# Optimization experiments

Measured on AMD Instinct MI355X. Metric: run time of the kernel, lower is better.

The kernel has to match this reference:

```python
import jax, jax.numpy as jnp
import numpy as np

NUM_HEADS = 16
HEAD_DIM = 64
EMBED_DIM = 1024
NEG_INF = -1e9
LENGTHS = np.array([1024, 512, 768, 896, 1024, 640, 384, 896], dtype=np.int32)


def rotate_half(x):
    d = x.shape[-1] // 2
    return jnp.concatenate([-x[..., d:], x[..., :d]], axis=-1)


def setup_inputs() -> dict:
    key = jax.random.key(0)
    ks = jax.random.split(key, 8)
    E, H, Dh = EMBED_DIM, NUM_HEADS, HEAD_DIM
    T = int(LENGTHS.sum())  # 6144 packed tokens
    hidden_states = jax.random.normal(ks[0], (T, E), jnp.float32)
    # RoPE tables: positions restart at 0 for each packed segment
    pos = np.concatenate([np.arange(l) for l in LENGTHS]).astype(np.float32)
    inv_freq = 1.0 / (10000.0 ** (np.arange(0, Dh, 2, dtype=np.float32) / Dh))
    freqs = pos[:, None] * inv_freq[None, :]           # [T, Dh/2]
    emb = np.concatenate([freqs, freqs], axis=-1)       # [T, Dh]
    cos = jnp.asarray(np.cos(emb), jnp.float32)
    sin = jnp.asarray(np.sin(emb), jnp.float32)
    s = 0.02
    Wq = jax.random.normal(ks[1], (E, E), jnp.float32) * s
    Wk = jax.random.normal(ks[2], (E, E), jnp.float32) * s
    Wv = jax.random.normal(ks[3], (E, E), jnp.float32) * s
    Wo = jax.random.normal(ks[4], (E, E), jnp.float32) * s
    bq = jnp.zeros((E,), jnp.float32)
    bv = jnp.zeros((E,), jnp.float32)
    bo = jnp.zeros((E,), jnp.float32)
    return dict(hidden_states=hidden_states, seq_len=jnp.asarray(LENGTHS),
                cos=cos, sin=sin, Wq=Wq, bq=bq, Wk=Wk, Wv=Wv, bv=bv, Wo=Wo, bo=bo)


def reference(hidden_states, seq_len, cos, sin, Wq, bq, Wk, Wv, bv, Wo, bo):
    T, E = hidden_states.shape
    H, Dh = NUM_HEADS, HEAD_DIM
    # q/k/v projections (k_proj has no bias, matching nn.Linear(bias=False))
    q = (hidden_states @ Wq.T + bq).reshape(T, H, Dh)
    k = (hidden_states @ Wk.T).reshape(T, H, Dh)
    v = (hidden_states @ Wv.T + bv).reshape(T, H, Dh)
    # rotary embedding, cos/sin broadcast over heads
    c = cos[:, None, :]
    s = sin[:, None, :]
    q = q * c + rotate_half(q) * s
    k = k * c + rotate_half(k) * s
    # unpack ragged -> padded [B, Lmax, H, Dh] (indices are static wrt data)
    lens = np.asarray(seq_len)
    B = lens.shape[0]
    Lmax = int(lens.max())
    cu = np.concatenate([[0], np.cumsum(lens)])
    pad_idx = cu[:-1, None] + np.arange(Lmax)[None, :]   # [B, Lmax]
    valid = np.arange(Lmax)[None, :] < lens[:, None]     # [B, Lmax]
    pad_idx = np.where(valid, pad_idx, 0)
    qp = q[pad_idx]  # [B, Lmax, H, Dh]
    kp = k[pad_idx]
    vp = v[pad_idx]
    # attention with causal + key-padding mask (equivalent to per-segment loop)
    scores = jnp.einsum('bqhd,bkhd->bhqk', qp, kp) / np.sqrt(Dh).astype(np.float32)
    causal = np.tril(np.ones((Lmax, Lmax), dtype=bool))
    mask = causal[None, None, :, :] & valid[:, None, None, :]
    scores = jnp.where(mask, scores, NEG_INF)
    probs = jax.nn.softmax(scores, axis=-1)
    out = jnp.einsum('bhqk,bkhd->bqhd', probs, vp).reshape(B, Lmax, E)
    # repack padded -> [T, E]
    b_ids = np.repeat(np.arange(B), lens)
    l_ids = np.concatenate([np.arange(l) for l in lens])
    packed = out[b_ids, l_ids]
    return packed @ Wo.T + bo
```

## Files before the change

### kernel.cpp

```cpp
#include <hip/hip_runtime.h>
#include <stdint.h>

typedef __bf16 bf16;
typedef __bf16 bf16x8 __attribute__((ext_vector_type(8)));
typedef __bf16 bf16x4 __attribute__((ext_vector_type(4)));
typedef float f32x4 __attribute__((ext_vector_type(4)));

#define T_TOT 6144
#define E_DIM 1024
#define NHEAD 16

__device__ __forceinline__ void gload16(const void* g, void* l) {
    __builtin_amdgcn_global_load_lds((const __attribute__((address_space(1))) void*)g,
                                     (__attribute__((address_space(3))) void*)l, 16, 0, 0);
}

__global__ __launch_bounds__(256) void cvt_all_kernel(const float* __restrict__ hs,
        const float* __restrict__ wq, const float* __restrict__ wk,
        const float* __restrict__ wv, const float* __restrict__ wo,
        bf16* __restrict__ hsb, bf16* __restrict__ wqb, bf16* __restrict__ wkb,
        bf16* __restrict__ wvb, bf16* __restrict__ wob) {
    const size_t TE = (size_t)T_TOT * E_DIM;
    const size_t EE = (size_t)E_DIM * E_DIM;
    size_t i = ((size_t)blockIdx.x * 256 + threadIdx.x) * 4;
    const float* src; bf16* dst; size_t off;
    if (i < TE)               { src = hs; dst = hsb; off = i; }
    else if (i < TE + EE)     { src = wq; dst = wqb; off = i - TE; }
    else if (i < TE + 2 * EE) { src = wk; dst = wkb; off = i - TE - EE; }
    else if (i < TE + 3 * EE) { src = wv; dst = wvb; off = i - TE - 2 * EE; }
    else                      { src = wo; dst = wob; off = i - TE - 3 * EE; }
    float4 v = *reinterpret_cast<const float4*>(src + off);
    union { bf16 h[4]; uint2 u; } pk;
    pk.h[0] = (bf16)v.x; pk.h[1] = (bf16)v.y; pk.h[2] = (bf16)v.z; pk.h[3] = (bf16)v.w;
    *reinterpret_cast<uint2*>(dst + off) = pk.u;
}

__global__ __launch_bounds__(256, 2) void qkv_gemm_kernel(
        const bf16* __restrict__ hsb,
        const bf16* __restrict__ wq, const bf16* __restrict__ wk, const bf16* __restrict__ wv,
        const float* __restrict__ bq, const float* __restrict__ bv,
        const float* __restrict__ cosb, const float* __restrict__ sinb,
        bf16* __restrict__ qo, bf16* __restrict__ ko, bf16* __restrict__ vto) {
    __shared__ bf16 As[192 * 64];
    __shared__ bf16 Bs[128 * 64];

    const int b    = blockIdx.x;
    const int swzi = (b & 7) * 96 + (b >> 3);
    const int bn   = swzi & 7;
    const int t1   = swzi >> 3;
    const int bm   = t1 & 31;
    const int z    = t1 >> 5;
    const bf16*  W    = (z == 0) ? wq : (z == 1) ? wk : wv;
    const float* bias = (z == 0) ? bq : (z == 1) ? nullptr : bv;

    const int tid  = threadIdx.x;
    const int lane = tid & 63;
    const int wid  = tid >> 6;
    const int l15  = lane & 15, l4 = lane >> 4;
    const int wr   = wid >> 1, wc = wid & 1;

    f32x4 acc[6][4] = {};

    const bf16* Ag = hsb + (size_t)bm * 192 * E_DIM;
    const bf16* Bg = W   + (size_t)bn * 128 * E_DIM;

    const int srow = tid >> 3, sc8 = (tid & 7) * 8;

    for (int k0 = 0; k0 < E_DIM; k0 += 64) {
        #pragma unroll
        for (int j = 0; j < 6; ++j)
            gload16(Ag + (size_t)(j * 32 + srow) * E_DIM + k0 + sc8,
                    As + (size_t)(j * 256 + wid * 64) * 8);
        #pragma unroll
        for (int j = 0; j < 4; ++j)
            gload16(Bg + (size_t)(j * 32 + srow) * E_DIM + k0 + sc8,
                    Bs + (size_t)(j * 256 + wid * 64) * 8);
        __syncthreads();

        bf16x8 bfr[4][2];
        #pragma unroll
        for (int n = 0; n < 4; ++n)
            #pragma unroll
            for (int ks = 0; ks < 2; ++ks)
                bfr[n][ks] = *reinterpret_cast<const bf16x8*>(
                    &Bs[(wc * 64 + n * 16 + l15) * 64 + (ks * 4 + l4) * 8]);
        #pragma unroll
        for (int m = 0; m < 6; ++m) {
            bf16x8 af0 = *reinterpret_cast<const bf16x8*>(
                &As[(wr * 96 + m * 16 + l15) * 64 + l4 * 8]);
            bf16x8 af1 = *reinterpret_cast<const bf16x8*>(
                &As[(wr * 96 + m * 16 + l15) * 64 + (4 + l4) * 8]);
            #pragma unroll
            for (int n = 0; n < 4; ++n) {
                acc[m][n] = __builtin_amdgcn_mfma_f32_16x16x32_bf16(af0, bfr[n][0], acc[m][n], 0, 0, 0);
                acc[m][n] = __builtin_amdgcn_mfma_f32_16x16x32_bf16(af1, bfr[n][1], acc[m][n], 0, 0, 0);
            }
        }
        __syncthreads();
    }

    const int colb = bn * 128 + wc * 64;
    if (z <= 1) {
        bf16* out = (z == 0) ? qo : ko;
        #pragma unroll
        for (int n = 0; n < 2; ++n) {
            const int col_lo = colb + n * 16 + l15;
            const int dlo    = n * 16 + l15;
            const float b_lo = bias ? bias[col_lo] : 0.0f;
            const float b_hi = bias ? bias[col_lo + 32] : 0.0f;
            #pragma unroll
            for (int m = 0; m < 6; ++m) {
                #pragma unroll
                for (int r = 0; r < 4; ++r) {
                    const int t = bm * 192 + wr * 96 + m * 16 + l4 * 4 + r;
                    const float c = cosb[t * 64 + dlo];
                    const float s = sinb[t * 64 + dlo];
                    const float lo = acc[m][n][r] + b_lo;
                    const float hi = acc[m][n + 2][r] + b_hi;
                    out[(size_t)t * E_DIM + col_lo]      = (bf16)(lo * c - hi * s);
                    out[(size_t)t * E_DIM + col_lo + 32] = (bf16)(hi * c + lo * s);
                }
            }
        }
    } else {
        #pragma unroll
        for (int n = 0; n < 4; ++n) {
            const int col  = colb + n * 16 + l15;
            const float bc = bias[col];
            #pragma unroll
            for (int m = 0; m < 6; ++m) {
                const int t0r = bm * 192 + wr * 96 + m * 16 + l4 * 4;
                bf16x4 pk;
                #pragma unroll
                for (int r = 0; r < 4; ++r)
                    pk[r] = (bf16)(acc[m][n][r] + bc);
                *reinterpret_cast<bf16x4*>(vto + (size_t)col * T_TOT + t0r) = pk;
            }
        }
    }
}

__global__ __launch_bounds__(256, 4) void out_gemm_kernel(
        const bf16* __restrict__ attnb, const bf16* __restrict__ wo,
        const float* __restrict__ bo, float* __restrict__ out) {
    __shared__ bf16 As[64 * 64];
    __shared__ bf16 Bs[128 * 64];
    const int b   = blockIdx.x;
    const int swz = (b & 7) * 96 + (b >> 3);
    const int bn  = swz & 7;
    const int bm  = swz >> 3;

    const int tid  = threadIdx.x;
    const int lane = tid & 63;
    const int wid  = tid >> 6;
    const int l15  = lane & 15, l4 = lane >> 4;
    const int wr   = wid >> 1, wc = wid & 1;

    f32x4 acc[2][4] = {};

    const bf16* Ag = attnb + (size_t)bm * 64 * E_DIM;
    const bf16* Bg = wo    + (size_t)bn * 128 * E_DIM;

    const int srow = tid >> 3, sc8 = (tid & 7) * 8;

    for (int k0 = 0; k0 < E_DIM; k0 += 64) {
        #pragma unroll
        for (int j = 0; j < 2; ++j)
            gload16(Ag + (size_t)(j * 32 + srow) * E_DIM + k0 + sc8,
                    As + (size_t)(j * 256 + wid * 64) * 8);
        #pragma unroll
        for (int j = 0; j < 4; ++j)
            gload16(Bg + (size_t)(j * 32 + srow) * E_DIM + k0 + sc8,
                    Bs + (size_t)(j * 256 + wid * 64) * 8);
        __syncthreads();

        bf16x8 bfr[4][2];
        #pragma unroll
        for (int n = 0; n < 4; ++n)
            #pragma unroll
            for (int ks = 0; ks < 2; ++ks)
                bfr[n][ks] = *reinterpret_cast<const bf16x8*>(
                    &Bs[(wc * 64 + n * 16 + l15) * 64 + (ks * 4 + l4) * 8]);
        #pragma unroll
        for (int m = 0; m < 2; ++m) {
            bf16x8 af0 = *reinterpret_cast<const bf16x8*>(
                &As[(wr * 32 + m * 16 + l15) * 64 + l4 * 8]);
            bf16x8 af1 = *reinterpret_cast<const bf16x8*>(
                &As[(wr * 32 + m * 16 + l15) * 64 + (4 + l4) * 8]);
            #pragma unroll
            for (int n = 0; n < 4; ++n) {
                acc[m][n] = __builtin_amdgcn_mfma_f32_16x16x32_bf16(af0, bfr[n][0], acc[m][n], 0, 0, 0);
                acc[m][n] = __builtin_amdgcn_mfma_f32_16x16x32_bf16(af1, bfr[n][1], acc[m][n], 0, 0, 0);
            }
        }
        __syncthreads();
    }

    #pragma unroll
    for (int n = 0; n < 4; ++n) {
        const int col  = bn * 128 + wc * 64 + n * 16 + l15;
        const float bc = bo[col];
        #pragma unroll
        for (int m = 0; m < 2; ++m) {
            const int rowb = bm * 64 + wr * 32 + m * 16 + l4 * 4;
            #pragma unroll
            for (int r = 0; r < 4; ++r)
                out[(size_t)(rowb + r) * E_DIM + col] = acc[m][n][r] + bc;
        }
    }
}

__device__ __forceinline__ void stage_kv(const bf16* __restrict__ kp, const bf16* __restrict__ vtp,
                                         bf16* kls, bf16* vls, int tok0, int h,
                                         int wid, int lane) {
    #pragma unroll
    for (int j = 0; j < 2; ++j) {
        const int c   = j * 256 + wid * 64 + lane;
        const int row = c >> 3;
        const int c8s = (c & 7) ^ (row & 7);
        gload16(kp  + (size_t)(tok0 + row) * E_DIM + h * 64 + c8s * 8,
                kls + (size_t)(j * 256 + wid * 64) * 8);
        gload16(vtp + (size_t)(h * 64 + row) * T_TOT + tok0 + c8s * 8,
                vls + (size_t)(j * 256 + wid * 64) * 8);
    }
}

__device__ __forceinline__ int swz(int j, int col8) {
    return j * 64 + ((col8 ^ (j & 7)) << 3);
}

__global__ __launch_bounds__(256, 3) void attn_kernel(const bf16* __restrict__ q,
                                                      const bf16* __restrict__ k,
                                                      const bf16* __restrict__ vt,
                                                      bf16* __restrict__ attn) {
    const int cu[9] = {0, 1024, 1536, 2304, 3200, 4224, 4864, 5248, 6144};
    __shared__ bf16 kls[2][64 * 64];
    __shared__ bf16 vls[2][64 * 64];
    __shared__ bf16 p_lds[4][16][72];
    const int h   = blockIdx.x & 15;
    const int qt  = blockIdx.x >> 4;
    const int tid = threadIdx.x, lane = tid & 63, wid = tid >> 6;
    const int l15 = lane & 15, l4 = lane >> 4;

    const int tq0 = qt * 64;
    int b = 0;
    #pragma unroll
    for (int i = 0; i < 8; ++i) if (tq0 >= cu[i + 1]) b = i + 1;
    const int q0  = tq0 + wid * 16;
    const int p0  = q0 - cu[b];
    const int p0b = tq0 - cu[b];
    const int nkt = (p0b >> 6) + 1;
    const int pq  = p0 + l15;

    bf16x8 qf[2];
    #pragma unroll
    for (int kk = 0; kk < 2; ++kk)
        qf[kk] = *reinterpret_cast<const bf16x8*>(
            q + (size_t)(q0 + l15) * E_DIM + h * 64 + kk * 32 + l4 * 8);

    f32x4 o[4] = {};
    float mcur = -1e30f, lcur = 0.0f;

    stage_kv(k, vt, kls[0], vls[0], cu[b], h, wid, lane);
    __syncthreads();

    for (int kt = 0; kt < nkt; ++kt) {
        const int cur = kt & 1;
        if (kt + 1 < nkt)
            stage_kv(k, vt, kls[cur ^ 1], vls[cur ^ 1], cu[b] + (kt + 1) * 64, h, wid, lane);

        const int j0 = kt * 64;
        const bool diag = (kt == nkt - 1);

        f32x4 s[4] = {};
        #pragma unroll
        for (int nt = 0; nt < 4; ++nt) {
            #pragma unroll
            for (int kk = 0; kk < 2; ++kk) {
                bf16x8 kf = *reinterpret_cast<const bf16x8*>(&kls[cur][swz(nt * 16 + l15, kk * 4 + l4)]);
                s[nt] = __builtin_amdgcn_mfma_f32_16x16x32_bf16(kf, qf[kk], s[nt], 0, 0, 0);
            }
        }

        float tmax = -1e30f;
        #pragma unroll
        for (int nt = 0; nt < 4; ++nt) {
            #pragma unroll
            for (int r = 0; r < 4; ++r) {
                float sv = s[nt][r] * 0.125f;
                if (diag) {
                    const int kp = j0 + nt * 16 + l4 * 4 + r;
                    sv = (kp <= pq) ? sv : -1e30f;
                }
                s[nt][r] = sv;
                tmax = fmaxf(tmax, sv);
            }
        }
        tmax = fmaxf(tmax, __shfl_xor(tmax, 16));
        tmax = fmaxf(tmax, __shfl_xor(tmax, 32));
        const float mnew  = fmaxf(mcur, tmax);
        const float alpha = __expf(mcur - mnew);

        float rs = 0.0f;
        #pragma unroll
        for (int nt = 0; nt < 4; ++nt) {
            bf16x4 pk;
            #pragma unroll
            for (int r = 0; r < 4; ++r) {
                float p = __expf(s[nt][r] - mnew);
                rs += p;
                pk[r] = (bf16)p;
            }
            *reinterpret_cast<bf16x4*>(&p_lds[wid][l15][nt * 16 + l4 * 4]) = pk;
        }
        rs += __shfl_xor(rs, 16);
        rs += __shfl_xor(rs, 32);
        lcur = lcur * alpha + rs;
        mcur = mnew;

        float ar[4];
        #pragma unroll
        for (int r = 0; r < 4; ++r) ar[r] = __shfl(alpha, l4 * 4 + r);
        #pragma unroll
        for (int nt = 0; nt < 4; ++nt)
            #pragma unroll
            for (int r = 0; r < 4; ++r) o[nt][r] *= ar[r];

        bf16x8 pf[2];
        #pragma unroll
        for (int kk = 0; kk < 2; ++kk)
            pf[kk] = *reinterpret_cast<const bf16x8*>(&p_lds[wid][l15][kk * 32 + l4 * 8]);

        #pragma unroll
        for (int nt = 0; nt < 4; ++nt) {
            #pragma unroll
            for (int kk = 0; kk < 2; ++kk) {
                bf16x8 vf = *reinterpret_cast<const bf16x8*>(&vls[cur][swz(nt * 16 + l15, kk * 4 + l4)]);
                o[nt] = __builtin_amdgcn_mfma_f32_16x16x32_bf16(pf[kk], vf, o[nt], 0, 0, 0);
            }
        }
        __syncthreads();
    }

    float rinv[4];
    #pragma unroll
    for (int r = 0; r < 4; ++r)
        rinv[r] = __builtin_amdgcn_rcpf(__shfl(lcur, l4 * 4 + r));
    #pragma unroll
    for (int nt = 0; nt < 4; ++nt) {
        #pragma unroll
        for (int r = 0; r < 4; ++r) {
            float val = o[nt][r] * rinv[r];
            attn[(size_t)(q0 + l4 * 4 + r) * E_DIM + h * 64 + nt * 16 + l15] = (bf16)val;
        }
    }
}

extern "C" void kernel_launch(void* const* d_in, const int* in_sizes, int n_in,
                              void* d_out, int out_size, void* d_ws, size_t ws_size,
                              hipStream_t stream) {
    const float* hs   = (const float*)d_in[0];
    const float* cosb = (const float*)d_in[2];
    const float* sinb = (const float*)d_in[3];
    const float* Wq   = (const float*)d_in[4];
    const float* bq   = (const float*)d_in[5];
    const float* Wk   = (const float*)d_in[6];
    const float* Wv   = (const float*)d_in[7];
    const float* bv   = (const float*)d_in[8];
    const float* Wo   = (const float*)d_in[9];
    const float* bo   = (const float*)d_in[10];

    const size_t TE = (size_t)T_TOT * E_DIM;
    const size_t EE = (size_t)E_DIM * E_DIM;

    char* w = (char*)d_ws;
    bf16* hsb   = (bf16*)w; w += TE * 2;
    bf16* wqb   = (bf16*)w; w += EE * 2;
    bf16* wkb   = (bf16*)w; w += EE * 2;
    bf16* wvb   = (bf16*)w; w += EE * 2;
    bf16* wob   = (bf16*)w; w += EE * 2;
    bf16* qb    = (bf16*)w; w += TE * 2;
    bf16* kb    = (bf16*)w; w += TE * 2;
    bf16* vtb   = (bf16*)w; w += TE * 2;
    bf16* attnb = (bf16*)w; w += TE * 2;

    const int cvt_blocks = (int)((TE + 4 * EE) / 4 / 256);
    cvt_all_kernel<<<cvt_blocks, 256, 0, stream>>>(hs, Wq, Wk, Wv, Wo, hsb, wqb, wkb, wvb, wob);

    qkv_gemm_kernel<<<768, 256, 0, stream>>>(hsb, wqb, wkb, wvb, bq, bv, cosb, sinb, qb, kb, vtb);

    attn_kernel<<<(T_TOT / 64) * NHEAD, 256, 0, stream>>>(qb, kb, vtb, attnb);

    out_gemm_kernel<<<768, 256, 0, stream>>>(attnb, wob, bo, (float*)d_out);
}
```

Before: 122.0 us.

## Use 192x192 QKV GEMM tiles spanning concatenated Q/K/V weights with BK=32

The fused QKV projection now treats Wq/Wk/Wv as one 3072-wide output and tiles it 192x192 instead of 192x128 per matrix. That cuts the grid from 768 to 512 blocks and raises arithmetic intensity per block. K-step depth drops from 64 to 32 so LDS use stays small, and each wave now holds 6x6 accumulators. The epilogue works out per 64-column head-pair which of Q, K or V it belongs to and applies RoPE or the transposed V store. The risks are higher register pressure, which may hurt occupancy under launch_bounds(256,2), twice as many K iterations with barriers, and a grid of 512 blocks that may fill the CUs less evenly.

```diff
diff --git a/kernel.cpp b/kernel.cpp
--- a/kernel.cpp
+++ b/kernel.cpp
@@ -41,17 +41,13 @@
         const float* __restrict__ bq, const float* __restrict__ bv,
         const float* __restrict__ cosb, const float* __restrict__ sinb,
         bf16* __restrict__ qo, bf16* __restrict__ ko, bf16* __restrict__ vto) {
-    __shared__ bf16 As[192 * 64];
-    __shared__ bf16 Bs[128 * 64];
+    __shared__ bf16 As[192 * 32];
+    __shared__ bf16 Bs[192 * 32];
 
     const int b    = blockIdx.x;
-    const int swzi = (b & 7) * 96 + (b >> 3);
-    const int bn   = swzi & 7;
-    const int t1   = swzi >> 3;
-    const int bm   = t1 & 31;
-    const int z    = t1 >> 5;
-    const bf16*  W    = (z == 0) ? wq : (z == 1) ? wk : wv;
-    const float* bias = (z == 0) ? bq : (z == 1) ? nullptr : bv;
+    const int swzi = (b & 7) * 64 + (b >> 3);
+    const int bn   = swzi & 15;
+    const int bm   = swzi >> 4;
 
     const int tid  = threadIdx.x;
     const int lane = tid & 63;
@@ -59,55 +55,58 @@
     const int l15  = lane & 15, l4 = lane >> 4;
     const int wr   = wid >> 1, wc = wid & 1;
 
-    f32x4 acc[6][4] = {};
+    f32x4 acc[6][6] = {};
 
     const bf16* Ag = hsb + (size_t)bm * 192 * E_DIM;
-    const bf16* Bg = W   + (size_t)bn * 128 * E_DIM;
-
-    const int srow = tid >> 3, sc8 = (tid & 7) * 8;
-
-    for (int k0 = 0; k0 < E_DIM; k0 += 64) {
-        #pragma unroll
-        for (int j = 0; j < 6; ++j)
-            gload16(Ag + (size_t)(j * 32 + srow) * E_DIM + k0 + sc8,
+    const bf16* Bpass[3];
+    #pragma unroll
+    for (int j = 0; j < 3; ++j) {
+        const int g0 = bn * 192 + j * 64;
+        const int z0 = g0 >> 10;
+        const bf16* Wz = (z0 == 0) ? wq : (z0 == 1) ? wk : wv;
+        Bpass[j] = Wz + (size_t)(g0 & 1023) * E_DIM;
+    }
+
+    const int srow = tid >> 2, sc4 = (tid & 3) * 8;
+
+    for (int k0 = 0; k0 < E_DIM; k0 += 32) {
+        #pragma unroll
+        for (int j = 0; j < 3; ++j)
+            gload16(Ag + (size_t)(j * 64 + srow) * E_DIM + k0 + sc4,
                     As + (size_t)(j * 256 + wid * 64) * 8);
         #pragma unroll
-        for (int j = 0; j < 4; ++j)
-            gload16(Bg + (size_t)(j * 32 + srow) * E_DIM + k0 + sc8,
+        for (int j = 0; j < 3; ++j)
+            gload16(Bpass[j] + (size_t)srow * E_DIM + k0 + sc4,
                     Bs + (size_t)(j * 256 + wid * 64) * 8);
         __syncthreads();
 
-        bf16x8 bfr[4][2];
-        #pragma unroll
-        for (int n = 0; n < 4; ++n)
-            #pragma unroll
-            for (int ks = 0; ks < 2; ++ks)
-                bfr[n][ks] = *reinterpret_cast<const bf16x8*>(
-                    &Bs[(wc * 64 + n * 16 + l15) * 64 + (ks * 4 + l4) * 8]);
+        bf16x8 bfr[6];
+        #pragma unroll
+        for (int n = 0; n < 6; ++n)
+            bfr[n] = *reinterpret_cast<const bf16x8*>(
+                &Bs[(n * 32 + wc * 16 + l15) * 32 + l4 * 8]);
         #pragma unroll
         for (int m = 0; m < 6; ++m) {
-            bf16x8 af0 = *reinterpret_cast<const bf16x8*>(
-                &As[(wr * 96 + m * 16 + l15) * 64 + l4 * 8]);
-            bf16x8 af1 = *reinterpret_cast<const bf16x8*>(
-                &As[(wr * 96 + m * 16 + l15) * 64 + (4 + l4) * 8]);
-            #pragma unroll
-            for (int n = 0; n < 4; ++n) {
-                acc[m][n] = __builtin_amdgcn_mfma_f32_16x16x32_bf16(af0, bfr[n][0], acc[m][n], 0, 0, 0);
-                acc[m][n] = __builtin_amdgcn_mfma_f32_16x16x32_bf16(af1, bfr[n][1], acc[m][n], 0, 0, 0);
-            }
-        }
-        __syncthreads();
-    }
-
-    const int colb = bn * 128 + wc * 64;
-    if (z <= 1) {
-        bf16* out = (z == 0) ? qo : ko;
-        #pragma unroll
-        for (int n = 0; n < 2; ++n) {
-            const int col_lo = colb + n * 16 + l15;
-            const int dlo    = n * 16 + l15;
-            const float b_lo = bias ? bias[col_lo] : 0.0f;
-            const float b_hi = bias ? bias[col_lo + 32] : 0.0f;
+            bf16x8 af = *reinterpret_cast<const bf16x8*>(
+                &As[(wr * 96 + m * 16 + l15) * 32 + l4 * 8]);
+            #pragma unroll
+            for (int n = 0; n < 6; ++n)
+                acc[m][n] = __builtin_amdgcn_mfma_f32_16x16x32_bf16(af, bfr[n], acc[m][n], 0, 0, 0);
+        }
+        __syncthreads();
+    }
+
+    const int dlo = wc * 16 + l15;
+    #pragma unroll
+    for (int np = 0; np < 3; ++np) {
+        const int n   = np * 2;
+        const int g   = bn * 192 + n * 32 + dlo;
+        const int z   = g >> 10;
+        const int c0  = g & 1023;
+        if (z <= 1) {
+            bf16* out = (z == 0) ? qo : ko;
+            const float b_lo = (z == 0) ? bq[c0] : 0.0f;
+            const float b_hi = (z == 0) ? bq[c0 + 32] : 0.0f;
             #pragma unroll
             for (int m = 0; m < 6; ++m) {
                 #pragma unroll
@@ -116,25 +115,25 @@
                     const float c = cosb[t * 64 + dlo];
                     const float s = sinb[t * 64 + dlo];
                     const float lo = acc[m][n][r] + b_lo;
-                    const float hi = acc[m][n + 2][r] + b_hi;
-                    out[(size_t)t * E_DIM + col_lo]      = (bf16)(lo * c - hi * s);
-                    out[(size_t)t * E_DIM + col_lo + 32] = (bf16)(hi * c + lo * s);
+                    const float hi = acc[m][n + 1][r] + b_hi;
+                    out[(size_t)t * E_DIM + c0]      = (bf16)(lo * c - hi * s);
+                    out[(size_t)t * E_DIM + c0 + 32] = (bf16)(hi * c + lo * s);
                 }
             }
-        }
-    } else {
-        #pragma unroll
-        for (int n = 0; n < 4; ++n) {
-            const int col  = colb + n * 16 + l15;
-            const float bc = bias[col];
+        } else {
+            const float b_lo = bv[c0];
+            const float b_hi = bv[c0 + 32];
             #pragma unroll
             for (int m = 0; m < 6; ++m) {
                 const int t0r = bm * 192 + wr * 96 + m * 16 + l4 * 4;
-                bf16x4 pk;
+                bf16x4 plo, phi;
                 #pragma unroll
-                for (int r = 0; r < 4; ++r)
-                    pk[r] = (bf16)(acc[m][n][r] + bc);
-                *reinterpret_cast<bf16x4*>(vto + (size_t)col * T_TOT + t0r) = pk;
+                for (int r = 0; r < 4; ++r) {
+                    plo[r] = (bf16)(acc[m][n][r] + b_lo);
+                    phi[r] = (bf16)(acc[m][n + 1][r] + b_hi);
+                }
+                *reinterpret_cast<bf16x4*>(vto + (size_t)c0 * T_TOT + t0r)        = plo;
+                *reinterpret_cast<bf16x4*>(vto + (size_t)(c0 + 32) * T_TOT + t0r) = phi;
             }
         }
     }
@@ -387,7 +386,7 @@
     const int cvt_blocks = (int)((TE + 4 * EE) / 4 / 256);
     cvt_all_kernel<<<cvt_blocks, 256, 0, stream>>>(hs, Wq, Wk, Wv, Wo, hsb, wqb, wkb, wvb, wob);
 
-    qkv_gemm_kernel<<<768, 256, 0, stream>>>(hsb, wqb, wkb, wvb, bq, bv, cosb, sinb, qb, kb, vtb);
+    qkv_gemm_kernel<<<512, 256, 0, stream>>>(hsb, wqb, wkb, wvb, bq, bv, cosb, sinb, qb, kb, vtb);
 
     attn_kernel<<<(T_TOT / 64) * NHEAD, 256, 0, stream>>>(qb, kb, vtb, attnb);
 
```

Result: no change. 122.2 us (+0.2%).

## Fold softmax scale into Q, lazily rescale accumulator, transpose PV output layout

Applied to the files above, without the earlier changes.

Pre-scales the Q fragments by 1/sqrt(d) once instead of scaling every score, and rescales the running output and sum only when the wave-wide max grows by more than a threshold. It also swaps the MFMA operand order for P·V so each lane holds a full query row's outputs, which removes the alpha and denominator shuffles and allows vectorized bf16x4 stores. The costs are an extra bf16 rounding of the scaled Q and exponent values that can run up to e^8 before a rescale, which could affect accuracy.

```diff
diff --git a/kernel.cpp b/kernel.cpp
--- a/kernel.cpp
+++ b/kernel.cpp
@@ -254,9 +254,13 @@
 
     bf16x8 qf[2];
     #pragma unroll
-    for (int kk = 0; kk < 2; ++kk)
-        qf[kk] = *reinterpret_cast<const bf16x8*>(
+    for (int kk = 0; kk < 2; ++kk) {
+        bf16x8 raw = *reinterpret_cast<const bf16x8*>(
             q + (size_t)(q0 + l15) * E_DIM + h * 64 + kk * 32 + l4 * 8);
+        #pragma unroll
+        for (int e = 0; e < 8; ++e)
+            qf[kk][e] = (bf16)((float)raw[e] * 0.125f);
+    }
 
     f32x4 o[4] = {};
     float mcur = -1e30f, lcur = 0.0f;
@@ -287,7 +291,7 @@
         for (int nt = 0; nt < 4; ++nt) {
             #pragma unroll
             for (int r = 0; r < 4; ++r) {
-                float sv = s[nt][r] * 0.125f;
+                float sv = s[nt][r];
                 if (diag) {
                     const int kp = j0 + nt * 16 + l4 * 4 + r;
                     sv = (kp <= pq) ? sv : -1e30f;
@@ -298,8 +302,17 @@
         }
         tmax = fmaxf(tmax, __shfl_xor(tmax, 16));
         tmax = fmaxf(tmax, __shfl_xor(tmax, 32));
-        const float mnew  = fmaxf(mcur, tmax);
-        const float alpha = __expf(mcur - mnew);
+
+        if (!__all(tmax <= mcur + 8.0f)) {
+            const float mnew  = fmaxf(mcur, tmax);
+            const float alpha = __expf(mcur - mnew);
+            #pragma unroll
+            for (int nt = 0; nt < 4; ++nt)
+                #pragma unroll
+                for (int r = 0; r < 4; ++r) o[nt][r] *= alpha;
+            lcur *= alpha;
+            mcur = mnew;
+        }
 
         float rs = 0.0f;
         #pragma unroll
@@ -307,7 +320,7 @@
             bf16x4 pk;
             #pragma unroll
             for (int r = 0; r < 4; ++r) {
-                float p = __expf(s[nt][r] - mnew);
+                float p = __expf(s[nt][r] - mcur);
                 rs += p;
                 pk[r] = (bf16)p;
             }
@@ -315,16 +328,7 @@
         }
         rs += __shfl_xor(rs, 16);
         rs += __shfl_xor(rs, 32);
-        lcur = lcur * alpha + rs;
-        mcur = mnew;
-
-        float ar[4];
-        #pragma unroll
-        for (int r = 0; r < 4; ++r) ar[r] = __shfl(alpha, l4 * 4 + r);
-        #pragma unroll
-        for (int nt = 0; nt < 4; ++nt)
-            #pragma unroll
-            for (int r = 0; r < 4; ++r) o[nt][r] *= ar[r];
+        lcur += rs;
 
         bf16x8 pf[2];
         #pragma unroll
@@ -336,23 +340,21 @@
             #pragma unroll
             for (int kk = 0; kk < 2; ++kk) {
                 bf16x8 vf = *reinterpret_cast<const bf16x8*>(&vls[cur][swz(nt * 16 + l15, kk * 4 + l4)]);
-                o[nt] = __builtin_amdgcn_mfma_f32_16x16x32_bf16(pf[kk], vf, o[nt], 0, 0, 0);
-            }
-        }
-        __syncthreads();
-    }
-
-    float rinv[4];
-    #pragma unroll
-    for (int r = 0; r < 4; ++r)
-        rinv[r] = __builtin_amdgcn_rcpf(__shfl(lcur, l4 * 4 + r));
+                o[nt] = __builtin_amdgcn_mfma_f32_16x16x32_bf16(vf, pf[kk], o[nt], 0, 0, 0);
+            }
+        }
+        __syncthreads();
+    }
+
+    const float rinv = __builtin_amdgcn_rcpf(lcur);
     #pragma unroll
     for (int nt = 0; nt < 4; ++nt) {
-        #pragma unroll
-        for (int r = 0; r < 4; ++r) {
-            float val = o[nt][r] * rinv[r];
-            attn[(size_t)(q0 + l4 * 4 + r) * E_DIM + h * 64 + nt * 16 + l15] = (bf16)val;
-        }
+        bf16x4 pk;
+        #pragma unroll
+        for (int r = 0; r < 4; ++r)
+            pk[r] = (bf16)(o[nt][r] * rinv);
+        *reinterpret_cast<bf16x4*>(
+            attn + (size_t)(q0 + l15) * E_DIM + h * 64 + nt * 16 + l4 * 4) = pk;
     }
 }
 
```

Result: faster. 118.6 us (-2.8%).
